# Kernel tuning notes

Measured on AMD Instinct MI355X. Metric: run time of the kernel, lower is better.

The kernel has to match this reference:

```python
import jax, jax.numpy as jnp
import numpy as np

N, E = 100000, 1600000
IN, HID, NCLS = 128, 128, 64


def setup_inputs() -> dict:
    key = jax.random.key(0)
    ks = jax.random.split(key, 8)
    x = jax.random.normal(ks[0], (N, IN), jnp.float32)
    edge_index = jax.random.randint(ks[1], (2, E), 0, N, dtype=jnp.int32)
    s1 = 1.0 / np.sqrt(IN)
    s2 = 1.0 / np.sqrt(HID)
    return {
        "x": x,
        "edge_index": edge_index,
        "Wl1": jax.random.uniform(ks[2], (IN, HID), jnp.float32, -s1, s1),
        "Wr1": jax.random.uniform(ks[3], (IN, HID), jnp.float32, -s1, s1),
        "b1": jnp.zeros((HID,), jnp.float32),
        "Wl2": jax.random.uniform(ks[4], (HID, NCLS), jnp.float32, -s2, s2),
        "Wr2": jax.random.uniform(ks[5], (HID, NCLS), jnp.float32, -s2, s2),
        "b2": jnp.zeros((NCLS,), jnp.float32),
    }


def _sage_conv(x, src, dst, inv_deg, Wl, Wr, b):
    # mean-aggregate neighbor features at each destination node (PyG SAGEConv)
    agg = jax.ops.segment_sum(x[src], dst, num_segments=N)  # [N, d]
    agg = agg * inv_deg[:, None]
    # out = lin_l(mean_j x_j) + lin_r(x_i); bias lives in lin_l
    return agg @ Wl + x @ Wr + b


def reference(x, edge_index, Wl1, Wr1, b1, Wl2, Wr2, b2):
    src, dst = edge_index[0], edge_index[1]
    deg = jax.ops.segment_sum(jnp.ones((E,), jnp.float32), dst, num_segments=N)
    inv_deg = 1.0 / jnp.maximum(deg, 1.0)
    h = _sage_conv(x, src, dst, inv_deg, Wl1, Wr1, b1)
    h = jax.nn.relu(h)
    # dropout is identity at inference (training=False)
    h = _sage_conv(h, src, dst, inv_deg, Wl2, Wr2, b2)
    return jax.nn.log_softmax(h, axis=1)
```

## Files before the change

kernel.cpp:

```cpp
#include <hip/hip_runtime.h>
#include <hip/hip_bf16.h>


typedef __attribute__((ext_vector_type(8))) short short8;
typedef __attribute__((ext_vector_type(4))) float f32x4;
typedef __attribute__((ext_vector_type(2))) float f32x2;

#define NPB 512
#define BCAP 16384
#define CHUNK 8192

__device__ __forceinline__ ushort f2bf(float f) {
    unsigned u = __float_as_uint(f);
    return (ushort)((u + 0x7fff + ((u >> 16) & 1)) >> 16);
}
__device__ __forceinline__ float bflo(unsigned v) { return __uint_as_float(v << 16); }
__device__ __forceinline__ float bfhi(unsigned v) { return __uint_as_float(v & 0xffff0000u); }
__device__ __forceinline__ unsigned pk4bf(float a, float b) {
    unsigned r;
    asm("v_cvt_pk_bf16_f32 %0, %1, %2" : "=v"(r) : "v"(a), "v"(b));
    return r;
}
__device__ __forceinline__ f32x2 pkadd(f32x2 a, f32x2 b) {
    f32x2 r;
    asm("v_pk_add_f32 %0, %1, %2" : "=v"(r) : "v"(a), "v"(b));
    return r;
}
__device__ __forceinline__ f32x2 shflx2(f32x2 v, int m) {
    f32x2 r; r[0] = __shfl_xor(v[0], m); r[1] = __shfl_xor(v[1], m); return r;
}

__device__ __forceinline__ void wfrag_one(const float* W, ushort* Wf, int i, int COLS) {
    int j = i & 7, m = (i >> 3) & 15, kc = (i >> 7) & 15, ct = i >> 11;
    Wf[i] = f2bf(W[(kc * 8 + j) * COLS + ct * 16 + m]);
}

__global__ void __launch_bounds__(512)
k0_cvtw(const float* __restrict__ Wl1, const float* __restrict__ Wr1,
        const float* __restrict__ Wl2, const float* __restrict__ Wr2,
        ushort* __restrict__ Wf_l1, ushort* __restrict__ Wf_r1,
        ushort* __restrict__ Wf_l2, ushort* __restrict__ Wf_r2) {
    int i = (int)blockIdx.x * 512 + (int)threadIdx.x;
    if (i < 16384)       wfrag_one(Wl1, Wf_l1, i, 128);
    else if (i < 32768)  wfrag_one(Wr1, Wf_r1, i - 16384, 128);
    else if (i < 40960)  wfrag_one(Wl2, Wf_l2, i - 32768, 64);
    else if (i < 49152)  wfrag_one(Wr2, Wf_r2, i - 40960, 64);
}

template <int CTOT>
__device__ __forceinline__ void stage_weights(const ushort* __restrict__ Wfl,
                                              const ushort* __restrict__ Wfr,
                                              ushort* dst, int tid) {
    constexpr int HALF = CTOT / 2;
    constexpr int ITERS = (CTOT * 2) / 8192;
#pragma unroll
    for (int r = 0; r < ITERS; ++r) {
        int u = r * 4096 + tid * 8;
        const ushort* s = (u < HALF) ? (Wfl + u) : (Wfr + (u - HALF));
        *(short8*)(dst + u) = *(const short8*)s;
    }
}

template <int COLS, bool F32IN>
__device__ __forceinline__ void proj_tile(int bid, int tid,
                            const void* __restrict__ xin,
                            const ushort* Wl, const ushort* Wr,
                            const float* __restrict__ bias,
                            unsigned char* __restrict__ p8, ushort* __restrict__ q, int N) {
    constexpr int CT = COLS / 16;
    int wave = tid >> 6, lane = tid & 63;
    int quad = lane >> 4, m = lane & 15;
    long row0 = (long)bid * 128 + wave * 16;
    long node = row0 + m;
    long arow = (node < N) ? node : (N - 1);

    f32x4 accp[CT], accq[CT];
#pragma unroll
    for (int ct = 0; ct < CT; ++ct) { accp[ct] = (f32x4)0.0f; accq[ct] = (f32x4)0.0f; }

#pragma unroll
    for (int kk = 0; kk < 128; kk += 32) {
        short8 b;
        if (F32IN) {
            const float* xf = (const float*)xin + arow * 128 + kk + quad * 8;
            float4 f0 = *(const float4*)xf;
            float4 f1 = *(const float4*)(xf + 4);
            union { short8 s; unsigned u[4]; } bu;
            bu.u[0] = pk4bf(f0.x, f0.y); bu.u[1] = pk4bf(f0.z, f0.w);
            bu.u[2] = pk4bf(f1.x, f1.y); bu.u[3] = pk4bf(f1.z, f1.w);
            b = bu.s;
        } else {
            b = *(const short8*)((const ushort*)xin + arow * 128 + kk + quad * 8);
        }
        int kc = (kk >> 3) + quad;
#pragma unroll
        for (int ct = 0; ct < CT; ++ct) {
            int boff = ((ct * 16 + kc) * 16 + m) * 8;
            short8 al = *(const short8*)(Wl + boff);
            short8 ar = *(const short8*)(Wr + boff);
            accp[ct] = __builtin_amdgcn_mfma_f32_16x16x32_bf16(al, b, accp[ct], 0, 0, 0);
            accq[ct] = __builtin_amdgcn_mfma_f32_16x16x32_bf16(ar, b, accq[ct], 0, 0, 0);
        }
    }

    if (node <= N) {
        unsigned msk = (node == N) ? 0u : ~0u;
#pragma unroll
        for (int ct = 0; ct < CT; ++ct) {
            int c0 = ct * 16 + quad * 4;
            float4 bv = *(const float4*)(bias + c0);
            float q0 = accq[ct][0] + bv.x, q1 = accq[ct][1] + bv.y;
            float q2 = accq[ct][2] + bv.z, q3 = accq[ct][3] + bv.w;
            unsigned w = (unsigned)__builtin_amdgcn_cvt_pk_fp8_f32(accp[ct][0], accp[ct][1], 0, false);
            w = (unsigned)__builtin_amdgcn_cvt_pk_fp8_f32(accp[ct][2], accp[ct][3], (int)w, true);
            *(unsigned*)(p8 + node * COLS + c0) = w & msk;
            uint2 qw; qw.x = pk4bf(q0, q1) & msk; qw.y = pk4bf(q2, q3) & msk;
            *(uint2*)(q + node * COLS + c0) = qw;
        }
    }
}

__global__ void __launch_bounds__(512, 4)
k1_scatter_proj1(const int* __restrict__ src, const int* __restrict__ dst,
                 int* __restrict__ bcount, unsigned* __restrict__ bbuf,
                 int E, int NSC, int N,
                 const float* __restrict__ x,
                 const ushort* __restrict__ Wfl, const ushort* __restrict__ Wfr,
                 const float* __restrict__ bias,
                 unsigned char* __restrict__ p8, ushort* __restrict__ q) {
    extern __shared__ char smem[];
    int tid = threadIdx.x;
    if ((int)blockIdx.x >= NSC) {
        ushort* wsm = (ushort*)smem;
        stage_weights<2 * 128 * 128>(Wfl, Wfr, wsm, tid);
        __syncthreads();
        proj_tile<128, true>((int)blockIdx.x - NSC, tid, x, wsm, wsm + 128 * 128,
                             bias, p8, q, N);
        return;
    }
    unsigned* entry = (unsigned*)smem;
    unsigned char* ebkt = (unsigned char*)(entry + CHUNK);
    int* lhist = (int*)(ebkt + CHUNK);
    int* lbase = lhist + 256;
    int* lcur  = lbase + 256;
    if (tid < 256) lhist[tid] = 0;
    __syncthreads();
    int e0 = blockIdx.x * CHUNK;
    int cnt = min(CHUNK, E - e0);
    int nv = cnt >> 2;
    for (int t = tid; t < nv; t += 512) {
        int4 d4 = ((const int4*)(dst + e0))[t];
        int4 s4 = ((const int4*)(src + e0))[t];
        int i = t * 4;
        int b0 = d4.x >> 9, b1 = d4.y >> 9, b2 = d4.z >> 9, b3 = d4.w >> 9;
        entry[i + 0] = ((unsigned)s4.x << 9) | (unsigned)(d4.x & 511);
        entry[i + 1] = ((unsigned)s4.y << 9) | (unsigned)(d4.y & 511);
        entry[i + 2] = ((unsigned)s4.z << 9) | (unsigned)(d4.z & 511);
        entry[i + 3] = ((unsigned)s4.w << 9) | (unsigned)(d4.w & 511);
        ebkt[i + 0] = (unsigned char)b0; ebkt[i + 1] = (unsigned char)b1;
        ebkt[i + 2] = (unsigned char)b2; ebkt[i + 3] = (unsigned char)b3;
        atomicAdd(&lhist[b0], 1); atomicAdd(&lhist[b1], 1);
        atomicAdd(&lhist[b2], 1); atomicAdd(&lhist[b3], 1);
    }
    for (int i = (nv << 2) + tid; i < cnt; i += 512) {
        int d = dst[e0 + i], s = src[e0 + i];
        int b = d >> 9;
        entry[i] = ((unsigned)s << 9) | (unsigned)(d & 511);
        ebkt[i] = (unsigned char)b;
        atomicAdd(&lhist[b], 1);
    }
    __syncthreads();
    if (tid < 256) {
        int h = lhist[tid];
        lbase[tid] = (h > 0) ? atomicAdd(&bcount[tid], h) : 0;
        lcur[tid] = 0;
    }
    __syncthreads();
    for (int i = tid; i < cnt; i += 512) {
        int b = ebkt[i];
        int o = atomicAdd(&lcur[b], 1);
        bbuf[(long)b * BCAP + lbase[b] + o] = entry[i];
    }
}

__global__ void __launch_bounds__(512, 4)
k2_csr(const unsigned* __restrict__ bbuf, const int* __restrict__ bcount,
       int* __restrict__ rsd,
       float* __restrict__ inv_deg, int* __restrict__ ssrc, int N) {
    extern __shared__ char smem[];
    int tid = threadIdx.x;
    int* sdeg = (int*)smem;
    int* lcur = sdeg + NPB;
    int* wsum = lcur + NPB;
    unsigned* ecache = (unsigned*)(wsum + 16);
    const int ECAPV = 3836;
    int b = blockIdx.x;
    int node0 = b * NPB;
    sdeg[tid] = 0;
    __syncthreads();
    int cnt = bcount[b];
    long base = (long)b * BCAP;
    const unsigned* bb = bbuf + base;
    int nv = cnt >> 2;
    int cnv = min(nv, ECAPV);
    for (int t = tid; t < nv; t += 512) {
        uint4 e = ((const uint4*)bb)[t];
        if (t < cnv) ((uint4*)ecache)[t] = e;
        atomicAdd(&sdeg[e.x & 511], 1);
        atomicAdd(&sdeg[e.y & 511], 1);
        atomicAdd(&sdeg[e.z & 511], 1);
        atomicAdd(&sdeg[e.w & 511], 1);
    }
    for (int i = (nv << 2) + tid; i < cnt; i += 512)
        atomicAdd(&sdeg[bb[i] & 511], 1);
    __syncthreads();
    int lane = tid & 63, wv = tid >> 6;
    int c0 = sdeg[tid];
    int dp = (c0 + 15) & ~15;
    int v = dp;
#pragma unroll
    for (int o = 1; o < 64; o <<= 1) {
        int t = __shfl_up(v, o);
        if (lane >= o) v += t;
    }
    if (lane == 63) wsum[wv] = v;
    __syncthreads();
    int add = 0;
    for (int w = 0; w < wv; ++w) add += wsum[w];
    int rs0 = v + add - dp;
    lcur[tid] = rs0;
    if (node0 + tid < N) {
        int2 rv; rv.x = (int)(base + rs0); rv.y = dp;
        *(int2*)(rsd + 2 * (node0 + tid)) = rv;
        inv_deg[node0 + tid] = 1.0f / (float)(c0 > 1 ? c0 : 1);
    }
    __syncthreads();
    for (int t = tid; t < cnv; t += 512) {
        uint4 e = ((const uint4*)ecache)[t];
        int p0 = atomicAdd(&lcur[e.x & 511], 1);
        int p1 = atomicAdd(&lcur[e.y & 511], 1);
        int p2 = atomicAdd(&lcur[e.z & 511], 1);
        int p3 = atomicAdd(&lcur[e.w & 511], 1);
        ssrc[base + p0] = (int)(e.x >> 9);
        ssrc[base + p1] = (int)(e.y >> 9);
        ssrc[base + p2] = (int)(e.z >> 9);
        ssrc[base + p3] = (int)(e.w >> 9);
    }
    for (int t = cnv + tid; t < nv; t += 512) {
        uint4 e = ((const uint4*)bb)[t];
        int p0 = atomicAdd(&lcur[e.x & 511], 1);
        int p1 = atomicAdd(&lcur[e.y & 511], 1);
        int p2 = atomicAdd(&lcur[e.z & 511], 1);
        int p3 = atomicAdd(&lcur[e.w & 511], 1);
        ssrc[base + p0] = (int)(e.x >> 9);
        ssrc[base + p1] = (int)(e.y >> 9);
        ssrc[base + p2] = (int)(e.z >> 9);
        ssrc[base + p3] = (int)(e.w >> 9);
    }
    for (int i = (nv << 2) + tid; i < cnt; i += 512) {
        unsigned w = bb[i];
        int pos = atomicAdd(&lcur[w & 511], 1);
        ssrc[base + pos] = (int)(w >> 9);
    }
    for (int i = c0; i < dp; ++i) ssrc[base + rs0 + i] = N;
    if (tid == 511) {
        int tot = v + add;
        for (int k = 0; k < 16; ++k) ssrc[base + tot + k] = N;
    }
}

__global__ void __launch_bounds__(256)
agg_relu_kernel(const unsigned char* __restrict__ p8,
                const ushort* __restrict__ q,
                const int* __restrict__ ssrc,
                const int* __restrict__ rsd,
                const float* __restrict__ inv_deg,
                ushort* __restrict__ hb, int N) {
    int wave = threadIdx.x >> 6, lane = threadIdx.x & 63;
    int n = blockIdx.x * 4 + wave;
    if (n >= N) return;
    int g = lane >> 4, lm = lane & 15;
    int2 rv = *(const int2*)(rsd + 2 * n);
    int start = rv.x, dp = rv.y;
    float iv = inv_deg[n];
    uint4 qv = make_uint4(0u, 0u, 0u, 0u);
    if (g == 0) qv = *(const uint4*)(q + (long)n * 128 + lm * 8);
    const int* sp = ssrc + start;
    const unsigned char* pb = p8 + lm * 8;
    f32x2 a0 = (f32x2)0.f, a1 = (f32x2)0.f, a2 = (f32x2)0.f, a3 = (f32x2)0.f;
    int4 s = *(const int4*)(sp + 4 * g);
    for (int j = 0; j < dp; j += 16) {
        uint2 v0 = *(const uint2*)(pb + (unsigned)s.x * 128u);
        uint2 v1 = *(const uint2*)(pb + (unsigned)s.y * 128u);
        uint2 v2 = *(const uint2*)(pb + (unsigned)s.z * 128u);
        uint2 v3 = *(const uint2*)(pb + (unsigned)s.w * 128u);
        s = *(const int4*)(sp + j + 16 + 4 * g);
        a0 = pkadd(a0, __builtin_amdgcn_cvt_pk_f32_fp8((int)v0.x, false));
        a1 = pkadd(a1, __builtin_amdgcn_cvt_pk_f32_fp8((int)v0.x, true));
        a2 = pkadd(a2, __builtin_amdgcn_cvt_pk_f32_fp8((int)v0.y, false));
        a3 = pkadd(a3, __builtin_amdgcn_cvt_pk_f32_fp8((int)v0.y, true));
        a0 = pkadd(a0, __builtin_amdgcn_cvt_pk_f32_fp8((int)v1.x, false));
        a1 = pkadd(a1, __builtin_amdgcn_cvt_pk_f32_fp8((int)v1.x, true));
        a2 = pkadd(a2, __builtin_amdgcn_cvt_pk_f32_fp8((int)v1.y, false));
        a3 = pkadd(a3, __builtin_amdgcn_cvt_pk_f32_fp8((int)v1.y, true));
        a0 = pkadd(a0, __builtin_amdgcn_cvt_pk_f32_fp8((int)v2.x, false));
        a1 = pkadd(a1, __builtin_amdgcn_cvt_pk_f32_fp8((int)v2.x, true));
        a2 = pkadd(a2, __builtin_amdgcn_cvt_pk_f32_fp8((int)v2.y, false));
        a3 = pkadd(a3, __builtin_amdgcn_cvt_pk_f32_fp8((int)v2.y, true));
        a0 = pkadd(a0, __builtin_amdgcn_cvt_pk_f32_fp8((int)v3.x, false));
        a1 = pkadd(a1, __builtin_amdgcn_cvt_pk_f32_fp8((int)v3.x, true));
        a2 = pkadd(a2, __builtin_amdgcn_cvt_pk_f32_fp8((int)v3.y, false));
        a3 = pkadd(a3, __builtin_amdgcn_cvt_pk_f32_fp8((int)v3.y, true));
    }
    a0 = pkadd(a0, shflx2(a0, 16)); a1 = pkadd(a1, shflx2(a1, 16));
    a2 = pkadd(a2, shflx2(a2, 16)); a3 = pkadd(a3, shflx2(a3, 16));
    a0 = pkadd(a0, shflx2(a0, 32)); a1 = pkadd(a1, shflx2(a1, 32));
    a2 = pkadd(a2, shflx2(a2, 32)); a3 = pkadd(a3, shflx2(a3, 32));
    if (g == 0) {
        float h0 = fmaxf(a0[0] * iv + bflo(qv.x), 0.f);
        float h1 = fmaxf(a0[1] * iv + bfhi(qv.x), 0.f);
        float h2 = fmaxf(a1[0] * iv + bflo(qv.y), 0.f);
        float h3 = fmaxf(a1[1] * iv + bfhi(qv.y), 0.f);
        float h4 = fmaxf(a2[0] * iv + bflo(qv.z), 0.f);
        float h5 = fmaxf(a2[1] * iv + bfhi(qv.z), 0.f);
        float h6 = fmaxf(a3[0] * iv + bflo(qv.w), 0.f);
        float h7 = fmaxf(a3[1] * iv + bfhi(qv.w), 0.f);
        uint4 hw;
        hw.x = pk4bf(h0, h1); hw.y = pk4bf(h2, h3);
        hw.z = pk4bf(h4, h5); hw.w = pk4bf(h6, h7);
        *(uint4*)(hb + (long)n * 128 + lm * 8) = hw;
    }
}

__global__ void __launch_bounds__(512, 4)
proj2_kernel(const ushort* __restrict__ hb,
             const ushort* __restrict__ Wfl, const ushort* __restrict__ Wfr,
             const float* __restrict__ bias,
             unsigned char* __restrict__ u8, ushort* __restrict__ v, int N) {
    __shared__ ushort wsm[2 * 64 * 128];
    stage_weights<2 * 64 * 128>(Wfl, Wfr, wsm, (int)threadIdx.x);
    __syncthreads();
    proj_tile<64, false>((int)blockIdx.x, (int)threadIdx.x, hb, wsm, wsm + 64 * 128,
                         bias, u8, v, N);
}

__global__ void __launch_bounds__(256)
agg_lsm_kernel(const unsigned char* __restrict__ u8,
               const ushort* __restrict__ v,
               const int* __restrict__ ssrc,
               const int* __restrict__ rsd,
               const float* __restrict__ inv_deg,
               float* __restrict__ out, int N) {
    int wave = threadIdx.x >> 6, lane = threadIdx.x & 63;
    int n = blockIdx.x * 4 + wave;
    if (n >= N) return;
    int g = lane >> 4, lm = lane & 15;
    int2 rv = *(const int2*)(rsd + 2 * n);
    int start = rv.x, dp = rv.y;
    float iv = inv_deg[n];
    uint2 vv2 = *(const uint2*)(v + (long)n * 64 + lm * 4);
    const int* sp = ssrc + start;
    const unsigned char* ub = u8 + lm * 4;
    f32x2 a0 = (f32x2)0.f, a1 = (f32x2)0.f;
    int4 s = *(const int4*)(sp + 4 * g);
    for (int j = 0; j < dp; j += 16) {
        unsigned v0 = *(const unsigned*)(ub + (unsigned)s.x * 64u);
        unsigned v1 = *(const unsigned*)(ub + (unsigned)s.y * 64u);
        unsigned v2 = *(const unsigned*)(ub + (unsigned)s.z * 64u);
        unsigned v3 = *(const unsigned*)(ub + (unsigned)s.w * 64u);
        s = *(const int4*)(sp + j + 16 + 4 * g);
        a0 = pkadd(a0, __builtin_amdgcn_cvt_pk_f32_fp8((int)v0, false));
        a1 = pkadd(a1, __builtin_amdgcn_cvt_pk_f32_fp8((int)v0, true));
        a0 = pkadd(a0, __builtin_amdgcn_cvt_pk_f32_fp8((int)v1, false));
        a1 = pkadd(a1, __builtin_amdgcn_cvt_pk_f32_fp8((int)v1, true));
        a0 = pkadd(a0, __builtin_amdgcn_cvt_pk_f32_fp8((int)v2, false));
        a1 = pkadd(a1, __builtin_amdgcn_cvt_pk_f32_fp8((int)v2, true));
        a0 = pkadd(a0, __builtin_amdgcn_cvt_pk_f32_fp8((int)v3, false));
        a1 = pkadd(a1, __builtin_amdgcn_cvt_pk_f32_fp8((int)v3, true));
    }
    a0 = pkadd(a0, shflx2(a0, 16)); a1 = pkadd(a1, shflx2(a1, 16));
    a0 = pkadd(a0, shflx2(a0, 32)); a1 = pkadd(a1, shflx2(a1, 32));

    float z0 = a0[0] * iv + bflo(vv2.x), z1 = a0[1] * iv + bfhi(vv2.x);
    float z2 = a1[0] * iv + bflo(vv2.y), z3 = a1[1] * iv + bfhi(vv2.y);
    float mx = fmaxf(fmaxf(z0, z1), fmaxf(z2, z3));
#pragma unroll
    for (int o = 8; o > 0; o >>= 1) mx = fmaxf(mx, __shfl_xor(mx, o));
    float e = (__expf(z0 - mx) + __expf(z1 - mx)) + (__expf(z2 - mx) + __expf(z3 - mx));
#pragma unroll
    for (int o = 8; o > 0; o >>= 1) e += __shfl_xor(e, o);
    float ls = mx + __logf(e);
    if (g == 0) {
        float4 o0;
        o0.x = z0 - ls; o0.y = z1 - ls; o0.z = z2 - ls; o0.w = z3 - ls;
        *(float4*)(out + (long)n * 64 + lm * 4) = o0;
    }
}

extern "C" void kernel_launch(void* const* d_in, const int* in_sizes, int n_in,
                              void* d_out, int out_size, void* d_ws, size_t ws_size,
                              hipStream_t stream) {
    const float* x   = (const float*)d_in[0];
    const int*   ei  = (const int*)d_in[1];
    const float* Wl1 = (const float*)d_in[2];
    const float* Wr1 = (const float*)d_in[3];
    const float* b1  = (const float*)d_in[4];
    const float* Wl2 = (const float*)d_in[5];
    const float* Wr2 = (const float*)d_in[6];
    const float* b2  = (const float*)d_in[7];

    const int N = in_sizes[0] / 128;
    const int E = in_sizes[1] / 2;
    const int* src = ei;
    const int* dst = ei + E;
    const int NB = (N + NPB - 1) / NPB;
    const int NSC = (E + CHUNK - 1) / CHUNK;

    size_t off = 0;
    auto take = [&](size_t nbytes) -> void* {
        void* ptr = (void*)((char*)d_ws + off);
        off += (nbytes + 255) & ~(size_t)255;
        return ptr;
    };
    int*      bcount    = (int*)take((size_t)NB * 4);
    unsigned* bbuf      = (unsigned*)take((size_t)NB * BCAP * 4);
    int*      rsd       = (int*)take((size_t)N * 8);
    float*    inv_deg   = (float*)take((size_t)N * 4);
    int*      ssrc      = (int*)take((size_t)NB * BCAP * 4);
    unsigned char* p8   = (unsigned char*)take((size_t)(N + 1) * 128);
    ushort*   q         = (ushort*)take((size_t)(N + 1) * 128 * 2);
    ushort*   hb        = (ushort*)take((size_t)N * 128 * 2);
    ushort*   Wf_l1     = (ushort*)take(128 * 128 * 2);
    ushort*   Wf_r1     = (ushort*)take(128 * 128 * 2);
    ushort*   Wf_l2     = (ushort*)take(64 * 128 * 2);
    ushort*   Wf_r2     = (ushort*)take(64 * 128 * 2);
    unsigned char* u8 = p8;
    ushort*        v  = q;
    (void)ws_size; (void)n_in; (void)out_size;

    static bool attr_set = false;
    if (!attr_set) {
        hipFuncSetAttribute((const void*)k1_scatter_proj1,
                            hipFuncAttributeMaxDynamicSharedMemorySize, 65536);
        hipFuncSetAttribute((const void*)k2_csr,
                            hipFuncAttributeMaxDynamicSharedMemorySize, 65536);
        attr_set = true;
    }

    hipMemsetAsync(bcount, 0, (size_t)NB * 4, stream);

    k0_cvtw<<<96, 512, 0, stream>>>(Wl1, Wr1, Wl2, Wr2, Wf_l1, Wf_r1, Wf_l2, Wf_r2);

    int P1 = (N + 127) / 128;
    k1_scatter_proj1<<<NSC + P1, 512, 65536, stream>>>(src, dst, bcount, bbuf,
                                                       E, NSC, N, x,
                                                       Wf_l1, Wf_r1, b1, p8, q);

    k2_csr<<<NB, 512, 65536, stream>>>(bbuf, bcount, rsd, inv_deg, ssrc, N);

    agg_relu_kernel<<<(N + 3) / 4, 256, 0, stream>>>(p8, q, ssrc, rsd, inv_deg, hb, N);

    proj2_kernel<<<(N + 127) / 128, 512, 0, stream>>>(hb, Wf_l2, Wf_r2, b2, u8, v, N);
    agg_lsm_kernel<<<(N + 3) / 4, 256, 0, stream>>>(u8, v, ssrc, rsd, inv_deg,
                                                    (float*)d_out, N);
}
```

Before: 246.9 us.

## Fuse CSR build, aggregation and layer-2 stages into one cooperative persistent kernel

Replaces four separate launches (CSR build, layer-1 aggregation with ReLU, layer-2 projection, final aggregation with log-softmax) with one cooperative kernel that uses grid-wide syncs between phases and grid-stride loops. The bcount memset is also folded into the weight-conversion kernel. This aims to remove launch gaps and per-kernel tails. In exchange, the grid is capped at the co-resident block count, which may reduce latency hiding in the gather phases. The CSR phase also drops the LDS edge cache, so the scatter pass re-reads bucket data from global memory.

```diff
diff --git a/kernel.cpp b/kernel.cpp
--- a/kernel.cpp
+++ b/kernel.cpp
@@ -1,5 +1,8 @@
 #include <hip/hip_runtime.h>
 #include <hip/hip_bf16.h>
+#include <hip/hip_cooperative_groups.h>
+
+namespace cg = cooperative_groups;
 
 
 typedef __attribute__((ext_vector_type(8))) short short8;
@@ -39,8 +42,11 @@
 k0_cvtw(const float* __restrict__ Wl1, const float* __restrict__ Wr1,
         const float* __restrict__ Wl2, const float* __restrict__ Wr2,
         ushort* __restrict__ Wf_l1, ushort* __restrict__ Wf_r1,
-        ushort* __restrict__ Wf_l2, ushort* __restrict__ Wf_r2) {
-    int i = (int)blockIdx.x * 512 + (int)threadIdx.x;
+        ushort* __restrict__ Wf_l2, ushort* __restrict__ Wf_r2,
+        int* __restrict__ bcount, int NB) {
+    int tid = (int)threadIdx.x;
+    if (blockIdx.x == 0 && tid < NB) bcount[tid] = 0;
+    int i = (int)blockIdx.x * 512 + tid;
     if (i < 16384)       wfrag_one(Wl1, Wf_l1, i, 128);
     else if (i < 32768)  wfrag_one(Wr1, Wf_r1, i - 16384, 128);
     else if (i < 40960)  wfrag_one(Wl2, Wf_l2, i - 32768, 64);
@@ -183,217 +189,204 @@
     }
 }
 
-__global__ void __launch_bounds__(512, 4)
-k2_csr(const unsigned* __restrict__ bbuf, const int* __restrict__ bcount,
-       int* __restrict__ rsd,
-       float* __restrict__ inv_deg, int* __restrict__ ssrc, int N) {
+__global__ void __launch_bounds__(512, 6)
+kc_fused(const unsigned* __restrict__ bbuf, const int* __restrict__ bcount,
+         int* __restrict__ rsd, float* __restrict__ inv_deg, int* __restrict__ ssrc,
+         int NBcsr, int N,
+         const unsigned char* __restrict__ p8, const ushort* __restrict__ q,
+         ushort* __restrict__ hb,
+         const ushort* __restrict__ Wfl2, const ushort* __restrict__ Wfr2,
+         const float* __restrict__ bias2,
+         unsigned char* __restrict__ u8, ushort* __restrict__ v,
+         float* __restrict__ out) {
     extern __shared__ char smem[];
+    cg::grid_group gg = cg::this_grid();
     int tid = threadIdx.x;
-    int* sdeg = (int*)smem;
-    int* lcur = sdeg + NPB;
-    int* wsum = lcur + NPB;
-    unsigned* ecache = (unsigned*)(wsum + 16);
-    const int ECAPV = 3836;
-    int b = blockIdx.x;
-    int node0 = b * NPB;
-    sdeg[tid] = 0;
-    __syncthreads();
-    int cnt = bcount[b];
-    long base = (long)b * BCAP;
-    const unsigned* bb = bbuf + base;
-    int nv = cnt >> 2;
-    int cnv = min(nv, ECAPV);
-    for (int t = tid; t < nv; t += 512) {
-        uint4 e = ((const uint4*)bb)[t];
-        if (t < cnv) ((uint4*)ecache)[t] = e;
-        atomicAdd(&sdeg[e.x & 511], 1);
-        atomicAdd(&sdeg[e.y & 511], 1);
-        atomicAdd(&sdeg[e.z & 511], 1);
-        atomicAdd(&sdeg[e.w & 511], 1);
-    }
-    for (int i = (nv << 2) + tid; i < cnt; i += 512)
-        atomicAdd(&sdeg[bb[i] & 511], 1);
-    __syncthreads();
-    int lane = tid & 63, wv = tid >> 6;
-    int c0 = sdeg[tid];
-    int dp = (c0 + 15) & ~15;
-    int v = dp;
-#pragma unroll
-    for (int o = 1; o < 64; o <<= 1) {
-        int t = __shfl_up(v, o);
-        if (lane >= o) v += t;
-    }
-    if (lane == 63) wsum[wv] = v;
-    __syncthreads();
-    int add = 0;
-    for (int w = 0; w < wv; ++w) add += wsum[w];
-    int rs0 = v + add - dp;
-    lcur[tid] = rs0;
-    if (node0 + tid < N) {
-        int2 rv; rv.x = (int)(base + rs0); rv.y = dp;
-        *(int2*)(rsd + 2 * (node0 + tid)) = rv;
-        inv_deg[node0 + tid] = 1.0f / (float)(c0 > 1 ? c0 : 1);
-    }
-    __syncthreads();
-    for (int t = tid; t < cnv; t += 512) {
-        uint4 e = ((const uint4*)ecache)[t];
-        int p0 = atomicAdd(&lcur[e.x & 511], 1);
-        int p1 = atomicAdd(&lcur[e.y & 511], 1);
-        int p2 = atomicAdd(&lcur[e.z & 511], 1);
-        int p3 = atomicAdd(&lcur[e.w & 511], 1);
-        ssrc[base + p0] = (int)(e.x >> 9);
-        ssrc[base + p1] = (int)(e.y >> 9);
-        ssrc[base + p2] = (int)(e.z >> 9);
-        ssrc[base + p3] = (int)(e.w >> 9);
-    }
-    for (int t = cnv + tid; t < nv; t += 512) {
-        uint4 e = ((const uint4*)bb)[t];
-        int p0 = atomicAdd(&lcur[e.x & 511], 1);
-        int p1 = atomicAdd(&lcur[e.y & 511], 1);
-        int p2 = atomicAdd(&lcur[e.z & 511], 1);
-        int p3 = atomicAdd(&lcur[e.w & 511], 1);
-        ssrc[base + p0] = (int)(e.x >> 9);
-        ssrc[base + p1] = (int)(e.y >> 9);
-        ssrc[base + p2] = (int)(e.z >> 9);
-        ssrc[base + p3] = (int)(e.w >> 9);
-    }
-    for (int i = (nv << 2) + tid; i < cnt; i += 512) {
-        unsigned w = bb[i];
-        int pos = atomicAdd(&lcur[w & 511], 1);
-        ssrc[base + pos] = (int)(w >> 9);
-    }
-    for (int i = c0; i < dp; ++i) ssrc[base + rs0 + i] = N;
-    if (tid == 511) {
-        int tot = v + add;
-        for (int k = 0; k < 16; ++k) ssrc[base + tot + k] = N;
-    }
-}
-
-__global__ void __launch_bounds__(256)
-agg_relu_kernel(const unsigned char* __restrict__ p8,
-                const ushort* __restrict__ q,
-                const int* __restrict__ ssrc,
-                const int* __restrict__ rsd,
-                const float* __restrict__ inv_deg,
-                ushort* __restrict__ hb, int N) {
-    int wave = threadIdx.x >> 6, lane = threadIdx.x & 63;
-    int n = blockIdx.x * 4 + wave;
-    if (n >= N) return;
-    int g = lane >> 4, lm = lane & 15;
-    int2 rv = *(const int2*)(rsd + 2 * n);
-    int start = rv.x, dp = rv.y;
-    float iv = inv_deg[n];
-    uint4 qv = make_uint4(0u, 0u, 0u, 0u);
-    if (g == 0) qv = *(const uint4*)(q + (long)n * 128 + lm * 8);
-    const int* sp = ssrc + start;
-    const unsigned char* pb = p8 + lm * 8;
-    f32x2 a0 = (f32x2)0.f, a1 = (f32x2)0.f, a2 = (f32x2)0.f, a3 = (f32x2)0.f;
-    int4 s = *(const int4*)(sp + 4 * g);
-    for (int j = 0; j < dp; j += 16) {
-        uint2 v0 = *(const uint2*)(pb + (unsigned)s.x * 128u);
-        uint2 v1 = *(const uint2*)(pb + (unsigned)s.y * 128u);
-        uint2 v2 = *(const uint2*)(pb + (unsigned)s.z * 128u);
-        uint2 v3 = *(const uint2*)(pb + (unsigned)s.w * 128u);
-        s = *(const int4*)(sp + j + 16 + 4 * g);
-        a0 = pkadd(a0, __builtin_amdgcn_cvt_pk_f32_fp8((int)v0.x, false));
-        a1 = pkadd(a1, __builtin_amdgcn_cvt_pk_f32_fp8((int)v0.x, true));
-        a2 = pkadd(a2, __builtin_amdgcn_cvt_pk_f32_fp8((int)v0.y, false));
-        a3 = pkadd(a3, __builtin_amdgcn_cvt_pk_f32_fp8((int)v0.y, true));
-        a0 = pkadd(a0, __builtin_amdgcn_cvt_pk_f32_fp8((int)v1.x, false));
-        a1 = pkadd(a1, __builtin_amdgcn_cvt_pk_f32_fp8((int)v1.x, true));
-        a2 = pkadd(a2, __builtin_amdgcn_cvt_pk_f32_fp8((int)v1.y, false));
-        a3 = pkadd(a3, __builtin_amdgcn_cvt_pk_f32_fp8((int)v1.y, true));
-        a0 = pkadd(a0, __builtin_amdgcn_cvt_pk_f32_fp8((int)v2.x, false));
-        a1 = pkadd(a1, __builtin_amdgcn_cvt_pk_f32_fp8((int)v2.x, true));
-        a2 = pkadd(a2, __builtin_amdgcn_cvt_pk_f32_fp8((int)v2.y, false));
-        a3 = pkadd(a3, __builtin_amdgcn_cvt_pk_f32_fp8((int)v2.y, true));
-        a0 = pkadd(a0, __builtin_amdgcn_cvt_pk_f32_fp8((int)v3.x, false));
-        a1 = pkadd(a1, __builtin_amdgcn_cvt_pk_f32_fp8((int)v3.x, true));
-        a2 = pkadd(a2, __builtin_amdgcn_cvt_pk_f32_fp8((int)v3.y, false));
-        a3 = pkadd(a3, __builtin_amdgcn_cvt_pk_f32_fp8((int)v3.y, true));
-    }
-    a0 = pkadd(a0, shflx2(a0, 16)); a1 = pkadd(a1, shflx2(a1, 16));
-    a2 = pkadd(a2, shflx2(a2, 16)); a3 = pkadd(a3, shflx2(a3, 16));
-    a0 = pkadd(a0, shflx2(a0, 32)); a1 = pkadd(a1, shflx2(a1, 32));
-    a2 = pkadd(a2, shflx2(a2, 32)); a3 = pkadd(a3, shflx2(a3, 32));
-    if (g == 0) {
-        float h0 = fmaxf(a0[0] * iv + bflo(qv.x), 0.f);
-        float h1 = fmaxf(a0[1] * iv + bfhi(qv.x), 0.f);
-        float h2 = fmaxf(a1[0] * iv + bflo(qv.y), 0.f);
-        float h3 = fmaxf(a1[1] * iv + bfhi(qv.y), 0.f);
-        float h4 = fmaxf(a2[0] * iv + bflo(qv.z), 0.f);
-        float h5 = fmaxf(a2[1] * iv + bfhi(qv.z), 0.f);
-        float h6 = fmaxf(a3[0] * iv + bflo(qv.w), 0.f);
-        float h7 = fmaxf(a3[1] * iv + bfhi(qv.w), 0.f);
-        uint4 hw;
-        hw.x = pk4bf(h0, h1); hw.y = pk4bf(h2, h3);
-        hw.z = pk4bf(h4, h5); hw.w = pk4bf(h6, h7);
-        *(uint4*)(hb + (long)n * 128 + lm * 8) = hw;
-    }
-}
-
-__global__ void __launch_bounds__(512, 4)
-proj2_kernel(const ushort* __restrict__ hb,
-             const ushort* __restrict__ Wfl, const ushort* __restrict__ Wfr,
-             const float* __restrict__ bias,
-             unsigned char* __restrict__ u8, ushort* __restrict__ v, int N) {
-    __shared__ ushort wsm[2 * 64 * 128];
-    stage_weights<2 * 64 * 128>(Wfl, Wfr, wsm, (int)threadIdx.x);
-    __syncthreads();
-    proj_tile<64, false>((int)blockIdx.x, (int)threadIdx.x, hb, wsm, wsm + 64 * 128,
-                         bias, u8, v, N);
-}
-
-__global__ void __launch_bounds__(256)
-agg_lsm_kernel(const unsigned char* __restrict__ u8,
-               const ushort* __restrict__ v,
-               const int* __restrict__ ssrc,
-               const int* __restrict__ rsd,
-               const float* __restrict__ inv_deg,
-               float* __restrict__ out, int N) {
-    int wave = threadIdx.x >> 6, lane = threadIdx.x & 63;
-    int n = blockIdx.x * 4 + wave;
-    if (n >= N) return;
-    int g = lane >> 4, lm = lane & 15;
-    int2 rv = *(const int2*)(rsd + 2 * n);
-    int start = rv.x, dp = rv.y;
-    float iv = inv_deg[n];
-    uint2 vv2 = *(const uint2*)(v + (long)n * 64 + lm * 4);
-    const int* sp = ssrc + start;
-    const unsigned char* ub = u8 + lm * 4;
-    f32x2 a0 = (f32x2)0.f, a1 = (f32x2)0.f;
-    int4 s = *(const int4*)(sp + 4 * g);
-    for (int j = 0; j < dp; j += 16) {
-        unsigned v0 = *(const unsigned*)(ub + (unsigned)s.x * 64u);
-        unsigned v1 = *(const unsigned*)(ub + (unsigned)s.y * 64u);
-        unsigned v2 = *(const unsigned*)(ub + (unsigned)s.z * 64u);
-        unsigned v3 = *(const unsigned*)(ub + (unsigned)s.w * 64u);
-        s = *(const int4*)(sp + j + 16 + 4 * g);
-        a0 = pkadd(a0, __builtin_amdgcn_cvt_pk_f32_fp8((int)v0, false));
-        a1 = pkadd(a1, __builtin_amdgcn_cvt_pk_f32_fp8((int)v0, true));
-        a0 = pkadd(a0, __builtin_amdgcn_cvt_pk_f32_fp8((int)v1, false));
-        a1 = pkadd(a1, __builtin_amdgcn_cvt_pk_f32_fp8((int)v1, true));
-        a0 = pkadd(a0, __builtin_amdgcn_cvt_pk_f32_fp8((int)v2, false));
-        a1 = pkadd(a1, __builtin_amdgcn_cvt_pk_f32_fp8((int)v2, true));
-        a0 = pkadd(a0, __builtin_amdgcn_cvt_pk_f32_fp8((int)v3, false));
-        a1 = pkadd(a1, __builtin_amdgcn_cvt_pk_f32_fp8((int)v3, true));
-    }
-    a0 = pkadd(a0, shflx2(a0, 16)); a1 = pkadd(a1, shflx2(a1, 16));
-    a0 = pkadd(a0, shflx2(a0, 32)); a1 = pkadd(a1, shflx2(a1, 32));
-
-    float z0 = a0[0] * iv + bflo(vv2.x), z1 = a0[1] * iv + bfhi(vv2.x);
-    float z2 = a1[0] * iv + bflo(vv2.y), z3 = a1[1] * iv + bfhi(vv2.y);
-    float mx = fmaxf(fmaxf(z0, z1), fmaxf(z2, z3));
-#pragma unroll
-    for (int o = 8; o > 0; o >>= 1) mx = fmaxf(mx, __shfl_xor(mx, o));
-    float e = (__expf(z0 - mx) + __expf(z1 - mx)) + (__expf(z2 - mx) + __expf(z3 - mx));
-#pragma unroll
-    for (int o = 8; o > 0; o >>= 1) e += __shfl_xor(e, o);
-    float ls = mx + __logf(e);
-    if (g == 0) {
-        float4 o0;
-        o0.x = z0 - ls; o0.y = z1 - ls; o0.z = z2 - ls; o0.w = z3 - ls;
-        *(float4*)(out + (long)n * 64 + lm * 4) = o0;
+    int bid = (int)blockIdx.x;
+    int G = (int)gridDim.x;
+    int wave = tid >> 6, lane = tid & 63;
+
+    if (bid < NBcsr) {
+        int* sdeg = (int*)smem;
+        int* lcur = sdeg + NPB;
+        int* wsum = lcur + NPB;
+        int b = bid;
+        int node0 = b * NPB;
+        sdeg[tid] = 0;
+        __syncthreads();
+        int cnt = bcount[b];
+        long base = (long)b * BCAP;
+        const unsigned* bb = bbuf + base;
+        int nv = cnt >> 2;
+        for (int t = tid; t < nv; t += 512) {
+            uint4 e = ((const uint4*)bb)[t];
+            atomicAdd(&sdeg[e.x & 511], 1);
+            atomicAdd(&sdeg[e.y & 511], 1);
+            atomicAdd(&sdeg[e.z & 511], 1);
+            atomicAdd(&sdeg[e.w & 511], 1);
+        }
+        for (int i = (nv << 2) + tid; i < cnt; i += 512)
+            atomicAdd(&sdeg[bb[i] & 511], 1);
+        __syncthreads();
+        int c0 = sdeg[tid];
+        int dp = (c0 + 15) & ~15;
+        int scan = dp;
+#pragma unroll
+        for (int o = 1; o < 64; o <<= 1) {
+            int t = __shfl_up(scan, o);
+            if (lane >= o) scan += t;
+        }
+        if (lane == 63) wsum[wave] = scan;
+        __syncthreads();
+        int add = 0;
+        for (int w = 0; w < wave; ++w) add += wsum[w];
+        int rs0 = scan + add - dp;
+        lcur[tid] = rs0;
+        if (node0 + tid < N) {
+            int2 rv; rv.x = (int)(base + rs0); rv.y = dp;
+            *(int2*)(rsd + 2 * (node0 + tid)) = rv;
+            inv_deg[node0 + tid] = 1.0f / (float)(c0 > 1 ? c0 : 1);
+        }
+        __syncthreads();
+        for (int t = tid; t < nv; t += 512) {
+            uint4 e = ((const uint4*)bb)[t];
+            int p0 = atomicAdd(&lcur[e.x & 511], 1);
+            int p1 = atomicAdd(&lcur[e.y & 511], 1);
+            int p2 = atomicAdd(&lcur[e.z & 511], 1);
+            int p3 = atomicAdd(&lcur[e.w & 511], 1);
+            ssrc[base + p0] = (int)(e.x >> 9);
+            ssrc[base + p1] = (int)(e.y >> 9);
+            ssrc[base + p2] = (int)(e.z >> 9);
+            ssrc[base + p3] = (int)(e.w >> 9);
+        }
+        for (int i = (nv << 2) + tid; i < cnt; i += 512) {
+            unsigned w = bb[i];
+            int pos = atomicAdd(&lcur[w & 511], 1);
+            ssrc[base + pos] = (int)(w >> 9);
+        }
+        for (int i = c0; i < dp; ++i) ssrc[base + rs0 + i] = N;
+        if (tid == 511) {
+            int tot = scan + add;
+            for (int k = 0; k < 16; ++k) ssrc[base + tot + k] = N;
+        }
+    }
+    __threadfence();
+    gg.sync();
+
+    {
+        int g = lane >> 4, lm = lane & 15;
+        const unsigned char* pb = p8 + lm * 8;
+        for (int n = bid * 8 + wave; n < N; n += G * 8) {
+            int2 rv2 = *(const int2*)(rsd + 2 * n);
+            int start = rv2.x, dp = rv2.y;
+            float iv = inv_deg[n];
+            uint4 qv = make_uint4(0u, 0u, 0u, 0u);
+            if (g == 0) qv = *(const uint4*)(q + (long)n * 128 + lm * 8);
+            const int* sp = ssrc + start;
+            f32x2 a0 = (f32x2)0.f, a1 = (f32x2)0.f, a2 = (f32x2)0.f, a3 = (f32x2)0.f;
+            int4 s = *(const int4*)(sp + 4 * g);
+            for (int j = 0; j < dp; j += 16) {
+                uint2 v0 = *(const uint2*)(pb + (unsigned)s.x * 128u);
+                uint2 v1 = *(const uint2*)(pb + (unsigned)s.y * 128u);
+                uint2 v2 = *(const uint2*)(pb + (unsigned)s.z * 128u);
+                uint2 v3 = *(const uint2*)(pb + (unsigned)s.w * 128u);
+                s = *(const int4*)(sp + j + 16 + 4 * g);
+                a0 = pkadd(a0, __builtin_amdgcn_cvt_pk_f32_fp8((int)v0.x, false));
+                a1 = pkadd(a1, __builtin_amdgcn_cvt_pk_f32_fp8((int)v0.x, true));
+                a2 = pkadd(a2, __builtin_amdgcn_cvt_pk_f32_fp8((int)v0.y, false));
+                a3 = pkadd(a3, __builtin_amdgcn_cvt_pk_f32_fp8((int)v0.y, true));
+                a0 = pkadd(a0, __builtin_amdgcn_cvt_pk_f32_fp8((int)v1.x, false));
+                a1 = pkadd(a1, __builtin_amdgcn_cvt_pk_f32_fp8((int)v1.x, true));
+                a2 = pkadd(a2, __builtin_amdgcn_cvt_pk_f32_fp8((int)v1.y, false));
+                a3 = pkadd(a3, __builtin_amdgcn_cvt_pk_f32_fp8((int)v1.y, true));
+                a0 = pkadd(a0, __builtin_amdgcn_cvt_pk_f32_fp8((int)v2.x, false));
+                a1 = pkadd(a1, __builtin_amdgcn_cvt_pk_f32_fp8((int)v2.x, true));
+                a2 = pkadd(a2, __builtin_amdgcn_cvt_pk_f32_fp8((int)v2.y, false));
+                a3 = pkadd(a3, __builtin_amdgcn_cvt_pk_f32_fp8((int)v2.y, true));
+                a0 = pkadd(a0, __builtin_amdgcn_cvt_pk_f32_fp8((int)v3.x, false));
+                a1 = pkadd(a1, __builtin_amdgcn_cvt_pk_f32_fp8((int)v3.x, true));
+                a2 = pkadd(a2, __builtin_amdgcn_cvt_pk_f32_fp8((int)v3.y, false));
+                a3 = pkadd(a3, __builtin_amdgcn_cvt_pk_f32_fp8((int)v3.y, true));
+            }
+            a0 = pkadd(a0, shflx2(a0, 16)); a1 = pkadd(a1, shflx2(a1, 16));
+            a2 = pkadd(a2, shflx2(a2, 16)); a3 = pkadd(a3, shflx2(a3, 16));
+            a0 = pkadd(a0, shflx2(a0, 32)); a1 = pkadd(a1, shflx2(a1, 32));
+            a2 = pkadd(a2, shflx2(a2, 32)); a3 = pkadd(a3, shflx2(a3, 32));
+            if (g == 0) {
+                float h0 = fmaxf(a0[0] * iv + bflo(qv.x), 0.f);
+                float h1 = fmaxf(a0[1] * iv + bfhi(qv.x), 0.f);
+                float h2 = fmaxf(a1[0] * iv + bflo(qv.y), 0.f);
+                float h3 = fmaxf(a1[1] * iv + bfhi(qv.y), 0.f);
+                float h4 = fmaxf(a2[0] * iv + bflo(qv.z), 0.f);
+                float h5 = fmaxf(a2[1] * iv + bfhi(qv.z), 0.f);
+                float h6 = fmaxf(a3[0] * iv + bflo(qv.w), 0.f);
+                float h7 = fmaxf(a3[1] * iv + bfhi(qv.w), 0.f);
+                uint4 hw;
+                hw.x = pk4bf(h0, h1); hw.y = pk4bf(h2, h3);
+                hw.z = pk4bf(h4, h5); hw.w = pk4bf(h6, h7);
+                *(uint4*)(hb + (long)n * 128 + lm * 8) = hw;
+            }
+        }
+    }
+    __threadfence();
+    gg.sync();
+
+    {
+        ushort* wsm = (ushort*)smem;
+        stage_weights<2 * 64 * 128>(Wfl2, Wfr2, wsm, tid);
+        __syncthreads();
+        int NT = (N + 127) / 128;
+        for (int t = bid; t < NT; t += G)
+            proj_tile<64, false>(t, tid, hb, wsm, wsm + 64 * 128, bias2, u8, v, N);
+    }
+    __threadfence();
+    gg.sync();
+
+    {
+        int g = lane >> 4, lm = lane & 15;
+        const unsigned char* ub = u8 + lm * 4;
+        for (int n = bid * 8 + wave; n < N; n += G * 8) {
+            int2 rv2 = *(const int2*)(rsd + 2 * n);
+            int start = rv2.x, dp = rv2.y;
+            float iv = inv_deg[n];
+            uint2 vv2 = *(const uint2*)(v + (long)n * 64 + lm * 4);
+            const int* sp = ssrc + start;
+            f32x2 a0 = (f32x2)0.f, a1 = (f32x2)0.f;
+            int4 s = *(const int4*)(sp + 4 * g);
+            for (int j = 0; j < dp; j += 16) {
+                unsigned v0 = *(const unsigned*)(ub + (unsigned)s.x * 64u);
+                unsigned v1 = *(const unsigned*)(ub + (unsigned)s.y * 64u);
+                unsigned v2 = *(const unsigned*)(ub + (unsigned)s.z * 64u);
+                unsigned v3 = *(const unsigned*)(ub + (unsigned)s.w * 64u);
+                s = *(const int4*)(sp + j + 16 + 4 * g);
+                a0 = pkadd(a0, __builtin_amdgcn_cvt_pk_f32_fp8((int)v0, false));
+                a1 = pkadd(a1, __builtin_amdgcn_cvt_pk_f32_fp8((int)v0, true));
+                a0 = pkadd(a0, __builtin_amdgcn_cvt_pk_f32_fp8((int)v1, false));
+                a1 = pkadd(a1, __builtin_amdgcn_cvt_pk_f32_fp8((int)v1, true));
+                a0 = pkadd(a0, __builtin_amdgcn_cvt_pk_f32_fp8((int)v2, false));
+                a1 = pkadd(a1, __builtin_amdgcn_cvt_pk_f32_fp8((int)v2, true));
+                a0 = pkadd(a0, __builtin_amdgcn_cvt_pk_f32_fp8((int)v3, false));
+                a1 = pkadd(a1, __builtin_amdgcn_cvt_pk_f32_fp8((int)v3, true));
+            }
+            a0 = pkadd(a0, shflx2(a0, 16)); a1 = pkadd(a1, shflx2(a1, 16));
+            a0 = pkadd(a0, shflx2(a0, 32)); a1 = pkadd(a1, shflx2(a1, 32));
+
+            float z0 = a0[0] * iv + bflo(vv2.x), z1 = a0[1] * iv + bfhi(vv2.x);
+            float z2 = a1[0] * iv + bflo(vv2.y), z3 = a1[1] * iv + bfhi(vv2.y);
+            float mx = fmaxf(fmaxf(z0, z1), fmaxf(z2, z3));
+#pragma unroll
+            for (int o = 8; o > 0; o >>= 1) mx = fmaxf(mx, __shfl_xor(mx, o));
+            float e = (__expf(z0 - mx) + __expf(z1 - mx)) +
+                      (__expf(z2 - mx) + __expf(z3 - mx));
+#pragma unroll
+            for (int o = 8; o > 0; o >>= 1) e += __shfl_xor(e, o);
+            float ls = mx + __logf(e);
+            if (g == 0) {
+                float4 o0;
+                o0.x = z0 - ls; o0.y = z1 - ls; o0.z = z2 - ls; o0.w = z3 - ls;
+                *(float4*)(out + (long)n * 64 + lm * 4) = o0;
+            }
+        }
     }
 }
 
@@ -436,31 +429,42 @@
     ushort*   Wf_r2     = (ushort*)take(64 * 128 * 2);
     unsigned char* u8 = p8;
     ushort*        v  = q;
+    float*    outp      = (float*)d_out;
     (void)ws_size; (void)n_in; (void)out_size;
 
-    static bool attr_set = false;
-    if (!attr_set) {
+    static int coop_grid = 0;
+    if (coop_grid == 0) {
         hipFuncSetAttribute((const void*)k1_scatter_proj1,
                             hipFuncAttributeMaxDynamicSharedMemorySize, 65536);
-        hipFuncSetAttribute((const void*)k2_csr,
+        hipFuncSetAttribute((const void*)kc_fused,
                             hipFuncAttributeMaxDynamicSharedMemorySize, 65536);
-        attr_set = true;
-    }
-
-    hipMemsetAsync(bcount, 0, (size_t)NB * 4, stream);
-
-    k0_cvtw<<<96, 512, 0, stream>>>(Wl1, Wr1, Wl2, Wr2, Wf_l1, Wf_r1, Wf_l2, Wf_r2);
+        int nb = 0;
+        hipOccupancyMaxActiveBlocksPerMultiprocessor(&nb, (const void*)kc_fused,
+                                                     512, 32768);
+        hipDeviceProp_t prop{};
+        int dev = 0;
+        hipGetDevice(&dev);
+        hipGetDeviceProperties(&prop, dev);
+        int g = nb * prop.multiProcessorCount;
+        if (g > 768) g = 768;
+        if (g < 256) g = 256;
+        coop_grid = g;
+    }
+
+    k0_cvtw<<<96, 512, 0, stream>>>(Wl1, Wr1, Wl2, Wr2, Wf_l1, Wf_r1, Wf_l2, Wf_r2,
+                                    bcount, NB);
 
     int P1 = (N + 127) / 128;
     k1_scatter_proj1<<<NSC + P1, 512, 65536, stream>>>(src, dst, bcount, bbuf,
                                                        E, NSC, N, x,
                                                        Wf_l1, Wf_r1, b1, p8, q);
 
-    k2_csr<<<NB, 512, 65536, stream>>>(bbuf, bcount, rsd, inv_deg, ssrc, N);
-
-    agg_relu_kernel<<<(N + 3) / 4, 256, 0, stream>>>(p8, q, ssrc, rsd, inv_deg, hb, N);
-
-    proj2_kernel<<<(N + 127) / 128, 512, 0, stream>>>(hb, Wf_l2, Wf_r2, b2, u8, v, N);
-    agg_lsm_kernel<<<(N + 3) / 4, 256, 0, stream>>>(u8, v, ssrc, rsd, inv_deg,
-                                                    (float*)d_out, N);
-}
+    int NBcsr = NB, n_arg = N;
+    void* args[] = { (void*)&bbuf, (void*)&bcount, (void*)&rsd, (void*)&inv_deg,
+                     (void*)&ssrc, (void*)&NBcsr, (void*)&n_arg,
+                     (void*)&p8, (void*)&q, (void*)&hb,
+                     (void*)&Wf_l2, (void*)&Wf_r2, (void*)&b2,
+                     (void*)&u8, (void*)&v, (void*)&outp };
+    hipLaunchCooperativeKernel((const void*)kc_fused, dim3(coop_grid), dim3(512),
+                               args, 32768, stream);
+}
```

Result: slower. 693.5 us (+180.9%).
